# Performance work log

Measured on AMD Instinct MI355X. Metric: run time of the kernel, lower is better.

## Reference

```python
import jax, jax.numpy as jnp
import numpy as np

D = 1024      # input_size
H = 16        # num_heads
HD = D // H   # head_dim
B, S = 8, 1024


def setup_inputs() -> dict:
    key = jax.random.key(0)
    ks = jax.random.split(key, 9)
    s = 1.0 / np.sqrt(D)
    return {
        "x": jax.random.normal(ks[0], (B, S, D), dtype=jnp.float32),
        "Wq": jax.random.uniform(ks[1], (D, D), jnp.float32, -s, s),
        "bq": jax.random.uniform(ks[2], (D,), jnp.float32, -s, s),
        "Wk": jax.random.uniform(ks[3], (D, D), jnp.float32, -s, s),
        "bk": jax.random.uniform(ks[4], (D,), jnp.float32, -s, s),
        "Wv": jax.random.uniform(ks[5], (D, D), jnp.float32, -s, s),
        "bv": jax.random.uniform(ks[6], (D,), jnp.float32, -s, s),
        "Wf": jax.random.uniform(ks[7], (D, D), jnp.float32, -s, s),
        "bf": jax.random.uniform(ks[8], (D,), jnp.float32, -s, s),
    }


def reference(x, Wq, bq, Wk, bk, Wv, bv, Wf, bf):
    b, s, d = x.shape
    # torch Linear: x @ W.T + b; split into heads -> [b, H, s, HD]
    def split(y):
        return y.reshape(b, s, H, HD).transpose(0, 2, 1, 3)
    q = split(x @ Wq.T + bq)
    k = split(x @ Wk.T + bk)
    v = split(x @ Wv.T + bv)
    scores = jnp.einsum("bhqd,bhkd->bhqk", q, k) / jnp.sqrt(jnp.float32(HD))
    probs = jax.nn.softmax(scores, axis=-1)
    ctx = jnp.einsum("bhqk,bhkd->bhqd", probs, v)
    ctx = ctx.transpose(0, 2, 1, 3).reshape(b, s, d)
    out = ctx @ Wf.T + bf
    return (out, probs)
```

## Files before the change

### kernel.cpp

```cpp
#include <hip/hip_runtime.h>

typedef __bf16 bf16;
typedef __bf16 bf16x4 __attribute__((ext_vector_type(4)));
typedef __bf16 bf16x8 __attribute__((ext_vector_type(8)));
typedef float  f32x4  __attribute__((ext_vector_type(4)));

constexpr int Bb = 8, Ss = 1024, Dd = 1024, Hh = 16, HDd = 64;
constexpr int Mm = Bb * Ss;
constexpr int Kk = 1024;

struct CastArgs {
  const float* src[5];
  bf16* dst[5];
  int cum[5];
};
__global__ void cast_all(CastArgs a, int tot) {
  int i = blockIdx.x * blockDim.x + threadIdx.x;
  if (i >= tot) return;
  int s, base;
  if (i < a.cum[0])      { s = 0; base = 0; }
  else if (i < a.cum[1]) { s = 1; base = a.cum[0]; }
  else if (i < a.cum[2]) { s = 2; base = a.cum[1]; }
  else if (i < a.cum[3]) { s = 3; base = a.cum[2]; }
  else                   { s = 4; base = a.cum[3]; }
  int j = i - base;
  float4 v = reinterpret_cast<const float4*>(a.src[s])[j];
  bf16x4 o = { (bf16)v.x, (bf16)v.y, (bf16)v.z, (bf16)v.w };
  reinterpret_cast<bf16x4*>(a.dst[s])[j] = o;
}

__device__ __forceinline__ void gemm_loop(const bf16* __restrict__ A, const bf16* __restrict__ Bm,
                                          int bm, int bn, unsigned char* As, unsigned char* Bs,
                                          int w, int lane, int l15, int g, f32x4 (&acc)[4][4]) {
  const bf16* srcA[4];
  const bf16* srcB[4];
#pragma unroll
  for (int i = 0; i < 4; ++i) {
    int gch = (w * 4 + i) * 64 + lane;
    int r = gch >> 3, c = gch & 7, cs = c ^ (r & 7);
    srcA[i] = A  + (size_t)(bm * 128 + r) * Kk + cs * 8;
    srcB[i] = Bm + (size_t)(bn * 128 + r) * Kk + cs * 8;
  }
  for (int kt = 0; kt < Kk / 64; ++kt) {
    __syncthreads();
#pragma unroll
    for (int i = 0; i < 4; ++i) {
      __builtin_amdgcn_global_load_lds(
          (const __attribute__((address_space(1))) void*)(srcA[i] + kt * 64),
          (__attribute__((address_space(3))) void*)(As + (w * 4 + i) * 1024), 16, 0, 0);
      __builtin_amdgcn_global_load_lds(
          (const __attribute__((address_space(1))) void*)(srcB[i] + kt * 64),
          (__attribute__((address_space(3))) void*)(Bs + (w * 4 + i) * 1024), 16, 0, 0);
    }
    __syncthreads();
#pragma unroll
    for (int kk = 0; kk < 2; ++kk) {
      const int kb = kk * 64 + g * 16;
      bf16x8 af[4], bfr[4];
#pragma unroll
      for (int mi = 0; mi < 4; ++mi) {
        int row = ((w >> 1) * 64) + mi * 16 + l15;
        af[mi] = *reinterpret_cast<const bf16x8*>(As + row * 128 + (kb ^ ((row & 7) << 4)));
      }
#pragma unroll
      for (int ni = 0; ni < 4; ++ni) {
        int row = ((w & 1) * 64) + ni * 16 + l15;
        bfr[ni] = *reinterpret_cast<const bf16x8*>(Bs + row * 128 + (kb ^ ((row & 7) << 4)));
      }
#pragma unroll
      for (int mi = 0; mi < 4; ++mi)
#pragma unroll
        for (int ni = 0; ni < 4; ++ni)
          acc[mi][ni] = __builtin_amdgcn_mfma_f32_16x16x32_bf16(af[mi], bfr[ni], acc[mi][ni], 0, 0, 0);
    }
  }
}

__global__ __launch_bounds__(256) void gemm_qkv(const bf16* __restrict__ x,
                                                const bf16* __restrict__ wq, const bf16* __restrict__ wk,
                                                const bf16* __restrict__ wv,
                                                const float* __restrict__ bq, const float* __restrict__ bk,
                                                const float* __restrict__ bv,
                                                bf16* __restrict__ Qo, bf16* __restrict__ Ko,
                                                bf16* __restrict__ Vto) {
  const int tid = threadIdx.x;
  const int lane = tid & 63;
  const int w = tid >> 6;
  const int l15 = lane & 15, g = lane >> 4;

  const int id = blockIdx.x;
  const int xcd = id & 7, slot = id >> 3;
  const int bmg = slot / 24, rem = slot % 24;
  const int bmx = xcd * 8 + bmg;
  const int bnx = rem & 7;
  const int z = rem >> 3;

  const bf16* A; const bf16* Bm; int bm, bn;
  if (z < 2) { A = x; Bm = z ? wk : wq; bm = bmx; bn = bnx; }
  else       { A = wv; Bm = x;          bm = bnx; bn = bmx; }

  __shared__ __align__(16) unsigned char As[128 * 128];
  __shared__ __align__(16) unsigned char Bs[128 * 128];
  f32x4 acc[4][4] = {};
  gemm_loop(A, Bm, bm, bn, As, Bs, w, lane, l15, g, acc);

  const int wr = (w >> 1) * 64, wc = (w & 1) * 64;
  if (z < 2) {
    const float* bias = z ? bk : bq;
    bf16* out = z ? Ko : Qo;
    const float scale = z ? 1.f : 0.125f * 1.44269504088896340736f;
#pragma unroll
    for (int ni = 0; ni < 4; ++ni) {
      int col = bn * 128 + wc + ni * 16 + l15;
      float bv_ = bias[col];
#pragma unroll
      for (int mi = 0; mi < 4; ++mi)
#pragma unroll
        for (int r = 0; r < 4; ++r) {
          int row = bm * 128 + wr + mi * 16 + g * 4 + r;
          float val = (acc[mi][ni][r] + bv_) * scale;
          size_t adr = ((size_t)((row >> 10) * Hh + (col >> 6)) * Ss + (row & 1023)) * HDd + (col & 63);
          out[adr] = (bf16)val;
        }
    }
  } else {
#pragma unroll
    for (int mi = 0; mi < 4; ++mi)
#pragma unroll
      for (int r = 0; r < 4; ++r) {
        int row = bm * 128 + wr + mi * 16 + g * 4 + r;
        float bv_ = bv[row];
#pragma unroll
        for (int ni = 0; ni < 4; ++ni) {
          int col = bn * 128 + wc + ni * 16 + l15;
          size_t adr = ((size_t)((col >> 10) * Hh + (row >> 6)) * HDd + (row & 63)) * Ss + (col & 1023);
          Vto[adr] = (bf16)(acc[mi][ni][r] + bv_);
        }
      }
  }
}

__global__ __launch_bounds__(256) void gemm_out(const bf16* __restrict__ A, const bf16* __restrict__ Bm,
                                                const float* __restrict__ bias, float* __restrict__ out) {
  const int tid = threadIdx.x;
  const int lane = tid & 63;
  const int w = tid >> 6;
  const int l15 = lane & 15, g = lane >> 4;
  const int id = blockIdx.x;
  const int xcd = id & 7, slot = id >> 3;
  const int bm = xcd * 8 + (slot >> 3);
  const int bn = slot & 7;
  __shared__ __align__(16) unsigned char As[128 * 128];
  __shared__ __align__(16) unsigned char Bs[128 * 128];
  f32x4 acc[4][4] = {};
  gemm_loop(A, Bm, bm, bn, As, Bs, w, lane, l15, g, acc);
  const int wr = (w >> 1) * 64, wc = (w & 1) * 64;
#pragma unroll
  for (int ni = 0; ni < 4; ++ni) {
    int col = bn * 128 + wc + ni * 16 + l15;
    float bv_ = bias[col];
#pragma unroll
    for (int mi = 0; mi < 4; ++mi)
#pragma unroll
      for (int r = 0; r < 4; ++r) {
        int row = bm * 128 + wr + mi * 16 + g * 4 + r;
        out[(size_t)row * Dd + col] = acc[mi][ni][r] + bv_;
      }
  }
}

#define WAITV(n) asm volatile("s_waitcnt vmcnt(" #n ")" ::: "memory")
#define PHASE_BAR { __builtin_amdgcn_s_barrier(); __builtin_amdgcn_sched_barrier(0); }

__global__ __launch_bounds__(512, 4) void attn_fused(const bf16* __restrict__ Q,
                                                     const bf16* __restrict__ Kt,
                                                     const bf16* __restrict__ Vt,
                                                     float* __restrict__ probs,
                                                     bf16* __restrict__ ctx) {
  const int tid = threadIdx.x;
  const int lane = tid & 63;
  const int w = tid >> 6;
  const int l15 = lane & 15, g = lane >> 4;
  const int bid = blockIdx.x;
  const int bh = (bid & 7) * 16 + ((bid >> 3) & 15);
  const int qt = bid >> 7;
  const int q0 = qt * 128 + w * 16;

  __shared__ __align__(16) unsigned char KV[4][16384];
  __shared__ __align__(16) bf16 Ps[8][16][40];

  bf16x8 qf0, qf1;
  {
    const bf16* qp = Q + ((size_t)bh * Ss + q0 + l15) * HDd + g * 8;
    qf0 = *reinterpret_cast<const bf16x8*>(qp);
    qf1 = *reinterpret_cast<const bf16x8*>(qp + 32);
  }
  const bf16* kbase = Kt + (size_t)bh * Ss * HDd;
  const bf16* vbase = Vt + (size_t)bh * HDd * Ss;

  const bf16* ksrc[2];
  const bf16* vsrc[2];
#pragma unroll
  for (int i = 0; i < 2; ++i) {
    int ch = i * 512 + tid;
    int kr = ch >> 3, kc = (ch & 7) ^ (kr & 7);
    ksrc[i] = kbase + (size_t)kr * HDd + kc * 8;
    int vr = ch >> 4, vc = (ch & 15) ^ (vr & 15);
    vsrc[i] = vbase + (size_t)vr * Ss + vc * 8;
  }

#define SK(slab, t)                                                                       \
  {                                                                                       \
    _Pragma("unroll") for (int i = 0; i < 2; ++i)                                         \
        __builtin_amdgcn_global_load_lds(                                                 \
            (const __attribute__((address_space(1))) void*)(ksrc[i] + (size_t)(t) * 128 * HDd), \
            (__attribute__((address_space(3))) void*)(KV[slab] + (i * 512 + w * 64) * 16),\
            16, 0, 0);                                                                    \
  }
#define SV(slab, t)                                                                       \
  {                                                                                       \
    _Pragma("unroll") for (int i = 0; i < 2; ++i)                                         \
        __builtin_amdgcn_global_load_lds(                                                 \
            (const __attribute__((address_space(1))) void*)(vsrc[i] + (t) * 128),         \
            (__attribute__((address_space(3))) void*)(KV[slab] + (i * 512 + w * 64) * 16),\
            16, 0, 0);                                                                    \
  }

  auto kread = [&](int slab, int nk, int half) -> bf16x8 {
    int row = nk * 16 + l15;
    int chunk = (half * 4 + g) ^ (l15 & 7);
    return *reinterpret_cast<const bf16x8*>(KV[slab] + row * 128 + chunk * 16);
  };
  auto vread = [&](int slab, int nkp, int ni) -> bf16x8 {
    int row = ni * 16 + l15;
    int chunk = (nkp * 4 + g) ^ l15;
    return *reinterpret_cast<const bf16x8*>(KV[slab] + row * 256 + chunk * 16);
  };

  float lr0 = 0.f, lr1 = 0.f, lr2 = 0.f, lr3 = 0.f;
  SK(0, 0); SK(1, 1); SK(2, 2);
  __builtin_amdgcn_sched_barrier(0);
  WAITV(4);
  PHASE_BAR;
  for (int kt = 0; kt < 8; ++kt) {
    if (kt <= 4)      { SK((kt + 3) & 3, kt + 3); }
    else if (kt == 7) { SK(0, 0); SV(2, 0); }
    __builtin_amdgcn_sched_barrier(0);
    const int ks = kt & 3;
#pragma unroll
    for (int nk = 0; nk < 8; ++nk) {
      f32x4 sc = {0.f, 0.f, 0.f, 0.f};
      bf16x8 k0 = kread(ks, nk, 0), k1 = kread(ks, nk, 1);
      __builtin_amdgcn_s_setprio(1);
      sc = __builtin_amdgcn_mfma_f32_16x16x32_bf16(k0, qf0, sc, 0, 0, 0);
      sc = __builtin_amdgcn_mfma_f32_16x16x32_bf16(k1, qf1, sc, 0, 0, 0);
      __builtin_amdgcn_s_setprio(0);
      lr0 += __builtin_amdgcn_exp2f(sc[0]);
      lr1 += __builtin_amdgcn_exp2f(sc[1]);
      lr2 += __builtin_amdgcn_exp2f(sc[2]);
      lr3 += __builtin_amdgcn_exp2f(sc[3]);
    }
    if (kt <= 4)      { WAITV(4); }
    else if (kt == 5) { WAITV(2); }
    else              { WAITV(0); }
    PHASE_BAR;
  }
  float lsum = (lr0 + lr1) + (lr2 + lr3);
  lsum += __shfl_xor(lsum, 16, 64);
  lsum += __shfl_xor(lsum, 32, 64);
  const float rl = 1.f / lsum;

  float* const prow = probs + ((size_t)bh * Ss + q0 + l15) * Ss;
  f32x4 cacc[4] = {};

  for (int kt = 0; kt < 8; ++kt) {
    if (kt < 7) { SK((kt + 1) & 1, kt + 1); SV(2 + ((kt + 1) & 1), kt + 1); }
    __builtin_amdgcn_sched_barrier(0);
    const int ks = kt & 1, vs = 2 + (kt & 1);
#pragma unroll
    for (int nkp = 0; nkp < 4; ++nkp) {
#pragma unroll
      for (int h = 0; h < 2; ++h) {
        int nk = nkp * 2 + h;
        f32x4 sc = {0.f, 0.f, 0.f, 0.f};
        bf16x8 k0 = kread(ks, nk, 0), k1 = kread(ks, nk, 1);
        __builtin_amdgcn_s_setprio(1);
        sc = __builtin_amdgcn_mfma_f32_16x16x32_bf16(k0, qf0, sc, 0, 0, 0);
        sc = __builtin_amdgcn_mfma_f32_16x16x32_bf16(k1, qf1, sc, 0, 0, 0);
        __builtin_amdgcn_s_setprio(0);
        f32x4 pv;
#pragma unroll
        for (int r = 0; r < 4; ++r) pv[r] = __builtin_amdgcn_exp2f(sc[r]) * rl;
        *reinterpret_cast<f32x4*>(prow + kt * 128 + nk * 16 + g * 4) = pv;
        bf16x4 pb = { (bf16)pv[0], (bf16)pv[1], (bf16)pv[2], (bf16)pv[3] };
        *reinterpret_cast<bf16x4*>(&Ps[w][l15][h * 16 + g * 4]) = pb;
      }
      bf16x8 pf = *reinterpret_cast<const bf16x8*>(&Ps[w][l15][g * 8]);
      bf16x8 vf0 = vread(vs, nkp, 0), vf1 = vread(vs, nkp, 1);
      bf16x8 vf2 = vread(vs, nkp, 2), vf3 = vread(vs, nkp, 3);
      __builtin_amdgcn_s_setprio(1);
      cacc[0] = __builtin_amdgcn_mfma_f32_16x16x32_bf16(pf, vf0, cacc[0], 0, 0, 0);
      cacc[1] = __builtin_amdgcn_mfma_f32_16x16x32_bf16(pf, vf1, cacc[1], 0, 0, 0);
      cacc[2] = __builtin_amdgcn_mfma_f32_16x16x32_bf16(pf, vf2, cacc[2], 0, 0, 0);
      cacc[3] = __builtin_amdgcn_mfma_f32_16x16x32_bf16(pf, vf3, cacc[3], 0, 0, 0);
      __builtin_amdgcn_s_setprio(0);
    }
    if (kt < 7) {
      WAITV(8);
      PHASE_BAR;
    }
  }
#undef SK
#undef SV

  const int bb = bh >> 4, hh = bh & 15;
#pragma unroll
  for (int ni = 0; ni < 4; ++ni)
#pragma unroll
    for (int r = 0; r < 4; ++r) {
      int q = q0 + g * 4 + r;
      ctx[((size_t)bb * Ss + q) * Dd + hh * 64 + ni * 16 + l15] = (bf16)cacc[ni][r];
    }
}

extern "C" void kernel_launch(void* const* d_in, const int* in_sizes, int n_in,
                              void* d_out, int out_size, void* d_ws, size_t ws_size,
                              hipStream_t stream) {
  (void)in_sizes; (void)n_in; (void)out_size; (void)ws_size;
  const float* x   = (const float*)d_in[0];
  const float* Wq  = (const float*)d_in[1];
  const float* bq  = (const float*)d_in[2];
  const float* Wk  = (const float*)d_in[3];
  const float* bk  = (const float*)d_in[4];
  const float* Wv  = (const float*)d_in[5];
  const float* bv  = (const float*)d_in[6];
  const float* Wf  = (const float*)d_in[7];
  const float* bfp = (const float*)d_in[8];

  char* ws = (char*)d_ws;
  size_t off = 0;
  auto alloc = [&](size_t n) { void* p = ws + off; off += (n + 255) & ~(size_t)255; return p; };
  bf16* xb   = (bf16*)alloc((size_t)Mm * Dd * 2);
  bf16* wqb  = (bf16*)alloc((size_t)Dd * Dd * 2);
  bf16* wkb  = (bf16*)alloc((size_t)Dd * Dd * 2);
  bf16* wvb  = (bf16*)alloc((size_t)Dd * Dd * 2);
  bf16* wfb  = (bf16*)alloc((size_t)Dd * Dd * 2);
  bf16* Qb   = (bf16*)alloc((size_t)Mm * Dd * 2);
  bf16* Kb   = (bf16*)alloc((size_t)Mm * Dd * 2);
  bf16* Vtb  = (bf16*)alloc((size_t)Mm * Dd * 2);
  bf16* ctxb = (bf16*)alloc((size_t)Mm * Dd * 2);

  CastArgs ca;
  ca.src[0] = x;  ca.dst[0] = xb;  int n0 = Mm * Dd / 4;
  ca.src[1] = Wq; ca.dst[1] = wqb; int nw = Dd * Dd / 4;
  ca.src[2] = Wk; ca.dst[2] = wkb;
  ca.src[3] = Wv; ca.dst[3] = wvb;
  ca.src[4] = Wf; ca.dst[4] = wfb;
  ca.cum[0] = n0; ca.cum[1] = n0 + nw; ca.cum[2] = n0 + 2 * nw;
  ca.cum[3] = n0 + 3 * nw; ca.cum[4] = n0 + 4 * nw;
  int tot = ca.cum[4];
  cast_all<<<(tot + 255) / 256, 256, 0, stream>>>(ca, tot);

  gemm_qkv<<<dim3(64 * 8 * 3), 256, 0, stream>>>(xb, wqb, wkb, wvb, bq, bk, bv, Qb, Kb, Vtb);

  float* probs = (float*)d_out + (size_t)Mm * Dd;
  attn_fused<<<dim3(Bb * Hh * 8), 512, 0, stream>>>(Qb, Kb, Vtb, probs, ctxb);

  gemm_out<<<dim3(64 * 8), 256, 0, stream>>>(ctxb, wfb, bfp, (float*)d_out);
}
```

Measured before the change: 261.5 us.

## Rewrite QKV GEMM with 256x256 tiles and pipelined direct-to-LDS loads

Replaces the 128x128, 256-thread QKV projection GEMM with a 256x256-tile, 512-thread kernel. Operands are staged with global_load_lds into double-buffered, swizzled LDS, using explicit vmcnt waits and barriers across eight phases per iteration so loads overlap MFMA work. The larger tile raises arithmetic intensity per loaded byte. In exchange it uses 128KB of LDS and more accumulator registers per thread, launches fewer blocks, and drops the XCD-aware block mapping in favour of a plain 3D grid.

Measured after the change: 288.5 us. +10.3%, slower.

```diff
diff --git a/kernel.cpp b/kernel.cpp
--- a/kernel.cpp
+++ b/kernel.cpp
@@ -8,6 +8,9 @@
 constexpr int Bb = 8, Ss = 1024, Dd = 1024, Hh = 16, HDd = 64;
 constexpr int Mm = Bb * Ss;
 constexpr int Kk = 1024;
+
+#define WAITV(n) asm volatile("s_waitcnt vmcnt(" #n ")" ::: "memory")
+#define PHASE_BAR { __builtin_amdgcn_s_barrier(); __builtin_amdgcn_sched_barrier(0); }
 
 struct CastArgs {
   const float* src[5];
@@ -76,65 +79,125 @@
   }
 }
 
-__global__ __launch_bounds__(256) void gemm_qkv(const bf16* __restrict__ x,
-                                                const bf16* __restrict__ wq, const bf16* __restrict__ wk,
-                                                const bf16* __restrict__ wv,
-                                                const float* __restrict__ bq, const float* __restrict__ bk,
-                                                const float* __restrict__ bv,
-                                                bf16* __restrict__ Qo, bf16* __restrict__ Ko,
-                                                bf16* __restrict__ Vto) {
+#define QSTG(DBUF, UNIT, SRCP, TOFF)                                                      \
+  { _Pragma("unroll") for (int i_ = 0; i_ < 2; ++i_)                                      \
+      __builtin_amdgcn_global_load_lds(                                                   \
+          (const __attribute__((address_space(1))) void*)(SRCP[i_] + (TOFF)),             \
+          (__attribute__((address_space(3))) void*)(L[DBUF][UNIT] + (i_ * 512 + w * 64) * 16), \
+          16, 0, 0); }
+
+#define QPH(CBUF, KS, NH, STG)                                                            \
+  {                                                                                       \
+    bf16x8 af[8], bfr[2];                                                                 \
+    _Pragma("unroll") for (int mf = 0; mf < 8; ++mf)                                      \
+      af[mf] = *reinterpret_cast<const bf16x8*>(L[CBUF][KS] + (arow + mf * 16) * 64 + ckoff); \
+    _Pragma("unroll") for (int nf = 0; nf < 2; ++nf)                                      \
+      bfr[nf] = *reinterpret_cast<const bf16x8*>(                                         \
+          L[CBUF][2 + KS] + (brow + (NH * 2 + nf) * 16) * 64 + ckoff);                    \
+    STG;                                                                                  \
+    __builtin_amdgcn_sched_barrier(0);                                                    \
+    __builtin_amdgcn_s_barrier();                                                         \
+    __builtin_amdgcn_s_setprio(1);                                                        \
+    _Pragma("unroll") for (int mf = 0; mf < 8; ++mf)                                      \
+      _Pragma("unroll") for (int nf = 0; nf < 2; ++nf)                                    \
+        acc[mf][NH * 2 + nf] = __builtin_amdgcn_mfma_f32_16x16x32_bf16(                   \
+            af[mf], bfr[nf], acc[mf][NH * 2 + nf], 0, 0, 0);                              \
+    __builtin_amdgcn_s_setprio(0);                                                        \
+    __builtin_amdgcn_s_barrier();                                                         \
+  }
+
+__global__ __launch_bounds__(512, 2) void gemm_qkv8(const bf16* __restrict__ x,
+                                                    const bf16* __restrict__ wq,
+                                                    const bf16* __restrict__ wk,
+                                                    const bf16* __restrict__ wv,
+                                                    const float* __restrict__ bq,
+                                                    const float* __restrict__ bk,
+                                                    const float* __restrict__ bv,
+                                                    bf16* __restrict__ Qo, bf16* __restrict__ Ko,
+                                                    bf16* __restrict__ Vto) {
   const int tid = threadIdx.x;
   const int lane = tid & 63;
   const int w = tid >> 6;
+  const int wm = w >> 2, wn = w & 3;
   const int l15 = lane & 15, g = lane >> 4;
-
-  const int id = blockIdx.x;
-  const int xcd = id & 7, slot = id >> 3;
-  const int bmg = slot / 24, rem = slot % 24;
-  const int bmx = xcd * 8 + bmg;
-  const int bnx = rem & 7;
-  const int z = rem >> 3;
+  const int z = blockIdx.z;
 
   const bf16* A; const bf16* Bm; int bm, bn;
-  if (z < 2) { A = x; Bm = z ? wk : wq; bm = bmx; bn = bnx; }
-  else       { A = wv; Bm = x;          bm = bnx; bn = bmx; }
-
-  __shared__ __align__(16) unsigned char As[128 * 128];
-  __shared__ __align__(16) unsigned char Bs[128 * 128];
-  f32x4 acc[4][4] = {};
-  gemm_loop(A, Bm, bm, bn, As, Bs, w, lane, l15, g, acc);
-
-  const int wr = (w >> 1) * 64, wc = (w & 1) * 64;
+  if (z < 2) { A = x; Bm = z ? wk : wq; bm = blockIdx.y; bn = blockIdx.x; }
+  else       { A = wv; Bm = x;          bm = blockIdx.x; bn = blockIdx.y; }
+
+  __shared__ __align__(16) unsigned char L[2][4][16384];
+
+  const bf16* srcA[2];
+  const bf16* srcB[2];
+#pragma unroll
+  for (int i = 0; i < 2; ++i) {
+    int ch = i * 512 + tid;
+    int r = ch >> 2, cl = ch & 3;
+    int cs = cl ^ (r & 3) ^ ((r >> 2) & 3);
+    srcA[i] = A  + (size_t)(bm * 256 + r) * Kk + cs * 8;
+    srcB[i] = Bm + (size_t)(bn * 256 + r) * Kk + cs * 8;
+  }
+  const int ckoff = ((g ^ (l15 & 3) ^ (l15 >> 2)) << 4);
+  const int arow = wm * 128 + l15;
+  const int brow = wn * 64 + l15;
+
+  f32x4 acc[8][4] = {};
+
+  QSTG(0, 0, srcA, 0);
+  QSTG(0, 2, srcB, 0);
+  QSTG(0, 1, srcA, 32);
+  QSTG(0, 3, srcB, 32);
+  QSTG(1, 0, srcA, 64);
+  QSTG(1, 2, srcB, 64);
+  __builtin_amdgcn_sched_barrier(0);
+  WAITV(8);
+  __builtin_amdgcn_s_barrier();
+
+  for (int j = 0; j < 8; ++j) {
+    const int t1o = (2 * j + 1) * 64, tn0 = (2 * j + 2) * 64, tn1 = (2 * j + 3) * 64;
+    const bool pf = (j < 7);
+    QPH(0, 0, 0, { QSTG(1, 1, srcA, t1o + 32); });
+    QPH(0, 0, 1, { QSTG(1, 3, srcB, t1o + 32); WAITV(8); });
+    QPH(0, 1, 0, { if (pf) QSTG(0, 0, srcA, tn0); });
+    QPH(0, 1, 1, { if (pf) { QSTG(0, 2, srcB, tn0); WAITV(8); } else { WAITV(0); } });
+    QPH(1, 0, 0, { if (pf) QSTG(0, 1, srcA, tn0 + 32); });
+    QPH(1, 0, 1, { if (pf) { QSTG(0, 3, srcB, tn0 + 32); WAITV(8); } else { WAITV(0); } });
+    QPH(1, 1, 0, { if (pf) QSTG(1, 0, srcA, tn1); });
+    QPH(1, 1, 1, { if (pf) { QSTG(1, 2, srcB, tn1); WAITV(8); } });
+  }
+
   if (z < 2) {
     const float* bias = z ? bk : bq;
     bf16* out = z ? Ko : Qo;
     const float scale = z ? 1.f : 0.125f * 1.44269504088896340736f;
 #pragma unroll
-    for (int ni = 0; ni < 4; ++ni) {
-      int col = bn * 128 + wc + ni * 16 + l15;
-      float bv_ = bias[col];
-#pragma unroll
-      for (int mi = 0; mi < 4; ++mi)
-#pragma unroll
-        for (int r = 0; r < 4; ++r) {
-          int row = bm * 128 + wr + mi * 16 + g * 4 + r;
-          float val = (acc[mi][ni][r] + bv_) * scale;
-          size_t adr = ((size_t)((row >> 10) * Hh + (col >> 6)) * Ss + (row & 1023)) * HDd + (col & 63);
+    for (int nf = 0; nf < 4; ++nf) {
+      int n = bn * 256 + wn * 64 + nf * 16 + l15;
+      float bv_ = bias[n];
+      int h = n >> 6, hd = n & 63;
+#pragma unroll
+      for (int mf = 0; mf < 8; ++mf)
+#pragma unroll
+        for (int rr = 0; rr < 4; ++rr) {
+          int m = bm * 256 + wm * 128 + mf * 16 + g * 4 + rr;
+          float val = (acc[mf][nf][rr] + bv_) * scale;
+          size_t adr = ((size_t)((m >> 10) * Hh + h) * Ss + (m & 1023)) * HDd + hd;
           out[adr] = (bf16)val;
         }
     }
   } else {
 #pragma unroll
-    for (int mi = 0; mi < 4; ++mi)
-#pragma unroll
-      for (int r = 0; r < 4; ++r) {
-        int row = bm * 128 + wr + mi * 16 + g * 4 + r;
-        float bv_ = bv[row];
-#pragma unroll
-        for (int ni = 0; ni < 4; ++ni) {
-          int col = bn * 128 + wc + ni * 16 + l15;
-          size_t adr = ((size_t)((col >> 10) * Hh + (row >> 6)) * HDd + (row & 63)) * Ss + (col & 1023);
-          Vto[adr] = (bf16)(acc[mi][ni][r] + bv_);
+    for (int mf = 0; mf < 8; ++mf)
+#pragma unroll
+      for (int rr = 0; rr < 4; ++rr) {
+        int m = bm * 256 + wm * 128 + mf * 16 + g * 4 + rr;
+        float bv_ = bv[m];
+#pragma unroll
+        for (int nf = 0; nf < 4; ++nf) {
+          int n = bn * 256 + wn * 64 + nf * 16 + l15;
+          size_t adr = ((size_t)((n >> 10) * Hh + (m >> 6)) * HDd + (m & 63)) * Ss + (n & 1023);
+          Vto[adr] = (bf16)(acc[mf][nf][rr] + bv_);
         }
       }
   }
@@ -169,9 +232,6 @@
   }
 }
 
-#define WAITV(n) asm volatile("s_waitcnt vmcnt(" #n ")" ::: "memory")
-#define PHASE_BAR { __builtin_amdgcn_s_barrier(); __builtin_amdgcn_sched_barrier(0); }
-
 __global__ __launch_bounds__(512, 4) void attn_fused(const bf16* __restrict__ Q,
                                                      const bf16* __restrict__ Kt,
                                                      const bf16* __restrict__ Vt,
@@ -361,7 +421,8 @@
   int tot = ca.cum[4];
   cast_all<<<(tot + 255) / 256, 256, 0, stream>>>(ca, tot);
 
-  gemm_qkv<<<dim3(64 * 8 * 3), 256, 0, stream>>>(xb, wqb, wkb, wvb, bq, bk, bv, Qb, Kb, Vtb);
+  gemm_qkv8<<<dim3(Dd / 256, Mm / 256, 3), 512, 0, stream>>>(xb, wqb, wkb, wvb, bq, bk, bv,
+                                                             Qb, Kb, Vtb);
 
   float* probs = (float*)d_out + (size_t)Mm * Dd;
   attn_fused<<<dim3(Bb * Hh * 8), 512, 0, stream>>>(Qb, Kb, Vtb, probs, ctxb);
```
